# Kernel optimization log

Hardware: AMD Instinct MI355X
Metric: run time of the kernel (lower is better)

The kernel has to match this reference:

```python
import jax, jax.numpy as jnp
import numpy as np

N_NODES = 10000
N_EDGES = 320000
D_IN = 256
D_OUT = 256


def setup_inputs() -> dict:
    key = jax.random.key(0)
    k1, k2, k3, k4, k5, k6 = jax.random.split(key, 6)
    feat = jax.random.normal(k1, (N_NODES, D_IN), dtype=jnp.float32)
    eweight = jax.random.uniform(k2, (N_EDGES, 1), dtype=jnp.float32)
    # Linear(in_dim*2 -> out_dim): weight [out, 2*in], bias [out]
    W = jax.random.normal(k3, (D_OUT, 2 * D_IN), dtype=jnp.float32) / np.sqrt(2 * D_IN)
    b = jax.random.normal(k4, (D_OUT,), dtype=jnp.float32) * 0.01
    src = jax.random.randint(k5, (N_EDGES,), 0, N_NODES, dtype=jnp.int64)
    dst = jax.random.randint(k6, (N_EDGES,), 0, N_NODES, dtype=jnp.int64)
    return {"feat": feat, "eweight": eweight, "W": W, "b": b, "src": src, "dst": dst}


def reference(feat, eweight, W, b, src, dst):
    n = feat.shape[0]
    # message: u_mul_e -> h[src] * ew   (broadcast [E,1] over [E,D])
    msg = feat[src] * eweight
    # mean reduce by destination: sum(msg) / in-degree
    agg = jax.ops.segment_sum(msg, dst, num_segments=n)
    deg = jax.ops.segment_sum(jnp.ones((src.shape[0],), dtype=feat.dtype), dst, num_segments=n)
    h_neigh = agg / jnp.maximum(deg, 1.0)[:, None]
    # concat aggregated with self features, then linear
    h = jnp.concatenate([h_neigh, feat], axis=-1)  # [N, 2*D]
    return h @ W.T + b
```

## Files before the change

kernel.cpp:

```cpp
#include <hip/hip_runtime.h>
#include <hip/hip_bf16.h>

#define N_NODES 10000
#define N_EDGES 320000
#define D 256
#define K_TOT 512
#define CAP 128

typedef __attribute__((ext_vector_type(8))) short bf16x8;
typedef __attribute__((ext_vector_type(4))) float f32x4;

__device__ __forceinline__ float bf2f(unsigned short u) {
  return __uint_as_float(((unsigned int)u) << 16);
}
__device__ __forceinline__ unsigned short f2bf(float f) {
  unsigned int x = __float_as_uint(f);
  unsigned int r = (x + 0x7fffu + ((x >> 16) & 1u)) >> 16;
  return (unsigned short)r;
}

#define FEAT_VECS (N_NODES * D / 8)
#define W_VECS    (D * K_TOT / 8)
#define CUR_VECS  (N_NODES / 4)
__global__ __launch_bounds__(256) void tobf16_kernel(
    const float* __restrict__ feat, const float* __restrict__ W,
    unsigned short* __restrict__ hcat, unsigned short* __restrict__ Wb,
    int* __restrict__ cursor) {
  int gid = blockIdx.x * 256 + threadIdx.x;
  const float* srcp;
  unsigned short* dstp;
  if (gid < FEAT_VECS) {
    int row = gid >> 5;
    int v = gid & 31;
    srcp = feat + (size_t)row * D + v * 8;
    dstp = hcat + (size_t)row * K_TOT + D + v * 8;
  } else if (gid < FEAT_VECS + W_VECS) {
    int g = gid - FEAT_VECS;
    int row = g >> 6;
    int v = g & 63;
    srcp = W + (size_t)row * K_TOT + v * 8;
    dstp = Wb + (size_t)row * K_TOT + v * 8;
  } else if (gid < FEAT_VECS + W_VECS + CUR_VECS) {
    int g = gid - (FEAT_VECS + W_VECS);
    reinterpret_cast<int4*>(cursor)[g] = make_int4(0, 0, 0, 0);
    return;
  } else {
    return;
  }
  float4 a = reinterpret_cast<const float4*>(srcp)[0];
  float4 b = reinterpret_cast<const float4*>(srcp)[1];
  ushort4 o0 = make_ushort4(f2bf(a.x), f2bf(a.y), f2bf(a.z), f2bf(a.w));
  ushort4 o1 = make_ushort4(f2bf(b.x), f2bf(b.y), f2bf(b.z), f2bf(b.w));
  reinterpret_cast<ushort4*>(dstp)[0] = o0;
  reinterpret_cast<ushort4*>(dstp)[1] = o1;
}

__global__ __launch_bounds__(256) void append_kernel(const int* __restrict__ src,
                                                     const int* __restrict__ dst,
                                                     const float* __restrict__ ew,
                                                     int* __restrict__ cursor,
                                                     int2* __restrict__ bucket) {
  int i = blockIdx.x * 256 + threadIdx.x;
  if (i < N_EDGES) {
    int d = dst[i];
    int pos = atomicAdd(&cursor[d], 1);
    if (pos < CAP)
      bucket[(size_t)d * CAP + pos] = make_int2(src[i], __float_as_int(ew[i]));
  }
}

__global__ __launch_bounds__(256) void agg_kernel(const int* __restrict__ cursor,
                                                  const int2* __restrict__ bucket,
                                                  unsigned short* __restrict__ hcat) {
  int node = (blockIdx.x * 256 + threadIdx.x) >> 6;
  int lane = threadIdx.x & 63;
  if (node >= N_NODES) return;
  int cnt = cursor[node];
  int end = min(cnt, CAP);
  const int2* bk = bucket + (size_t)node * CAP;
  float acc0 = 0.f, acc1 = 0.f, acc2 = 0.f, acc3 = 0.f;
  int i = 0;
  for (; i + 4 <= end; i += 4) {
    int4 e01 = *reinterpret_cast<const int4*>(bk + i);
    int4 e23 = *reinterpret_cast<const int4*>(bk + i + 2);
    ushort4 v0 = *reinterpret_cast<const ushort4*>(hcat + (size_t)e01.x * K_TOT + D + lane * 4);
    ushort4 v1 = *reinterpret_cast<const ushort4*>(hcat + (size_t)e01.z * K_TOT + D + lane * 4);
    ushort4 v2 = *reinterpret_cast<const ushort4*>(hcat + (size_t)e23.x * K_TOT + D + lane * 4);
    ushort4 v3 = *reinterpret_cast<const ushort4*>(hcat + (size_t)e23.z * K_TOT + D + lane * 4);
    float w0 = __int_as_float(e01.y), w1 = __int_as_float(e01.w);
    float w2 = __int_as_float(e23.y), w3 = __int_as_float(e23.w);
    acc0 += bf2f(v0.x) * w0; acc1 += bf2f(v0.y) * w0; acc2 += bf2f(v0.z) * w0; acc3 += bf2f(v0.w) * w0;
    acc0 += bf2f(v1.x) * w1; acc1 += bf2f(v1.y) * w1; acc2 += bf2f(v1.z) * w1; acc3 += bf2f(v1.w) * w1;
    acc0 += bf2f(v2.x) * w2; acc1 += bf2f(v2.y) * w2; acc2 += bf2f(v2.z) * w2; acc3 += bf2f(v2.w) * w2;
    acc0 += bf2f(v3.x) * w3; acc1 += bf2f(v3.y) * w3; acc2 += bf2f(v3.z) * w3; acc3 += bf2f(v3.w) * w3;
  }
  for (; i < end; ++i) {
    int2 sw = bk[i];
    ushort4 v = *reinterpret_cast<const ushort4*>(hcat + (size_t)sw.x * K_TOT + D + lane * 4);
    float w = __int_as_float(sw.y);
    acc0 += bf2f(v.x) * w; acc1 += bf2f(v.y) * w; acc2 += bf2f(v.z) * w; acc3 += bf2f(v.w) * w;
  }
  float inv = 1.0f / fmaxf((float)cnt, 1.0f);
  ushort4 o = make_ushort4(f2bf(acc0 * inv), f2bf(acc1 * inv),
                           f2bf(acc2 * inv), f2bf(acc3 * inv));
  *reinterpret_cast<ushort4*>(hcat + (size_t)node * K_TOT + lane * 4) = o;
}

#define GBM 128
#define GBN 64
#define GBK 64
#define LPAD 72

__global__ __launch_bounds__(256) void gemm_kernel(
    const unsigned short* __restrict__ hcat, const unsigned short* __restrict__ Wb,
    const float* __restrict__ bias, float* __restrict__ out) {
  __shared__ unsigned short As[GBM][LPAD];
  __shared__ unsigned short Bs[GBN][LPAD];

  int row0 = blockIdx.x * GBM;
  int col0 = blockIdx.y * GBN;
  int t = threadIdx.x;
  int lane = t & 63;
  int w = t >> 6;
  int wr = w >> 1;
  int wc = w & 1;
  int lhi = lane >> 4;
  int llo = lane & 15;

  f32x4 acc[4][2];
  #pragma unroll
  for (int m = 0; m < 4; ++m)
    #pragma unroll
    for (int n = 0; n < 2; ++n) acc[m][n] = (f32x4){0.f, 0.f, 0.f, 0.f};

  for (int k0 = 0; k0 < K_TOT; k0 += GBK) {
    #pragma unroll
    for (int it = 0; it < 4; ++it) {
      int idx = t + it * 256;
      int r = idx >> 3;
      int kv = (idx & 7) * 8;
      int row = row0 + r;
      uint4 v = make_uint4(0, 0, 0, 0);
      if (row < N_NODES)
        v = *reinterpret_cast<const uint4*>(hcat + (size_t)row * K_TOT + k0 + kv);
      *reinterpret_cast<uint4*>(&As[r][kv]) = v;
    }
    #pragma unroll
    for (int it = 0; it < 2; ++it) {
      int idx = t + it * 256;
      int c = idx >> 3;
      int kv = (idx & 7) * 8;
      uint4 v = *reinterpret_cast<const uint4*>(Wb + (size_t)(col0 + c) * K_TOT + k0 + kv);
      *reinterpret_cast<uint4*>(&Bs[c][kv]) = v;
    }
    __syncthreads();

    #pragma unroll
    for (int ks = 0; ks < 2; ++ks) {
      int ak = ks * 32 + lhi * 8;
      bf16x8 a[4], b[2];
      #pragma unroll
      for (int m = 0; m < 4; ++m)
        a[m] = *reinterpret_cast<const bf16x8*>(&As[wr * 64 + m * 16 + llo][ak]);
      #pragma unroll
      for (int n = 0; n < 2; ++n)
        b[n] = *reinterpret_cast<const bf16x8*>(&Bs[wc * 32 + n * 16 + llo][ak]);
      #pragma unroll
      for (int m = 0; m < 4; ++m)
        #pragma unroll
        for (int n = 0; n < 2; ++n)
          acc[m][n] = __builtin_amdgcn_mfma_f32_16x16x32_bf16(a[m], b[n], acc[m][n], 0, 0, 0);
    }
    __syncthreads();
  }

  #pragma unroll
  for (int m = 0; m < 4; ++m) {
    #pragma unroll
    for (int n = 0; n < 2; ++n) {
      int col = col0 + wc * 32 + n * 16 + llo;
      float bv = bias[col];
      #pragma unroll
      for (int r = 0; r < 4; ++r) {
        int orow = row0 + wr * 64 + m * 16 + lhi * 4 + r;
        if (orow < N_NODES)
          out[(size_t)orow * D + col] = acc[m][n][r] + bv;
      }
    }
  }
}

extern "C" void kernel_launch(void* const* d_in, const int* in_sizes, int n_in,
                              void* d_out, int out_size, void* d_ws, size_t ws_size,
                              hipStream_t stream) {
  const float* feat = (const float*)d_in[0];
  const float* ew   = (const float*)d_in[1];
  const float* W    = (const float*)d_in[2];
  const float* bias = (const float*)d_in[3];
  const int*   src  = (const int*)d_in[4];
  const int*   dst  = (const int*)d_in[5];
  float* out = (float*)d_out;

  char* ws = (char*)d_ws;
  unsigned short* hcat = (unsigned short*)ws;  ws += (size_t)N_NODES * K_TOT * sizeof(unsigned short);
  unsigned short* Wb   = (unsigned short*)ws;  ws += (size_t)D * K_TOT * sizeof(unsigned short);
  int* cursor   = (int*)ws;                    ws += N_NODES * sizeof(int);
  int2* bucket  = (int2*)ws;                   ws += (size_t)N_NODES * CAP * sizeof(int2);

  tobf16_kernel<<<(FEAT_VECS + W_VECS + CUR_VECS + 255) / 256, 256, 0, stream>>>(
      feat, W, hcat, Wb, cursor);
  append_kernel<<<(N_EDGES + 255) / 256, 256, 0, stream>>>(src, dst, ew, cursor, bucket);
  agg_kernel<<<(N_NODES * 64 + 255) / 256, 256, 0, stream>>>(cursor, bucket, hcat);

  dim3 grid((N_NODES + GBM - 1) / GBM, D / GBN);
  gemm_kernel<<<grid, 256, 0, stream>>>(hcat, Wb, bias, out);
}
```

Baseline: 76.92 us.

## Fuse all four stages into one cooperative persistent kernel with grid syncs

Replaces the four separate launches (bf16 conversion, edge bucketing, aggregation, GEMM) with a single cooperative kernel of 628 blocks. The blocks loop over each stage in grid-stride fashion and call grid.sync between stages. The GEMM tile shrinks to 64x64 so that 157x4 tiles map one-to-one onto the blocks. The goal is to remove per-launch overhead and the gaps between kernels. The cost is grid-wide barriers, occupancy limits on the persistent grid (launch bounds of 3 blocks), and a smaller GEMM tile with less reuse.

```diff
diff --git a/kernel.cpp b/kernel.cpp
--- a/kernel.cpp
+++ b/kernel.cpp
@@ -1,5 +1,8 @@
 #include <hip/hip_runtime.h>
 #include <hip/hip_bf16.h>
+#include <hip/hip_cooperative_groups.h>
+
+namespace cg = cooperative_groups;
 
 #define N_NODES 10000
 #define N_EDGES 320000
@@ -7,6 +10,9 @@
 #define K_TOT 512
 #define CAP 128
 
+#define GRID_BLKS 628
+#define NTHREADS (GRID_BLKS * 256)
+
 typedef __attribute__((ext_vector_type(8))) short bf16x8;
 typedef __attribute__((ext_vector_type(4))) float f32x4;
 
@@ -22,169 +28,177 @@
 #define FEAT_VECS (N_NODES * D / 8)
 #define W_VECS    (D * K_TOT / 8)
 #define CUR_VECS  (N_NODES / 4)
-__global__ __launch_bounds__(256) void tobf16_kernel(
-    const float* __restrict__ feat, const float* __restrict__ W,
+#define P0_TOT    (FEAT_VECS + W_VECS + CUR_VECS)
+
+#define GBM 64
+#define GBN 64
+#define GBK 64
+#define LPAD 72
+#define MTILES 157
+
+__global__ __launch_bounds__(256, 3) void fused_kernel(
+    const float* __restrict__ feat, const float* __restrict__ ew,
+    const float* __restrict__ W, const float* __restrict__ bias,
+    const int* __restrict__ src, const int* __restrict__ dst,
     unsigned short* __restrict__ hcat, unsigned short* __restrict__ Wb,
-    int* __restrict__ cursor) {
-  int gid = blockIdx.x * 256 + threadIdx.x;
-  const float* srcp;
-  unsigned short* dstp;
-  if (gid < FEAT_VECS) {
-    int row = gid >> 5;
-    int v = gid & 31;
-    srcp = feat + (size_t)row * D + v * 8;
-    dstp = hcat + (size_t)row * K_TOT + D + v * 8;
-  } else if (gid < FEAT_VECS + W_VECS) {
-    int g = gid - FEAT_VECS;
-    int row = g >> 6;
-    int v = g & 63;
-    srcp = W + (size_t)row * K_TOT + v * 8;
-    dstp = Wb + (size_t)row * K_TOT + v * 8;
-  } else if (gid < FEAT_VECS + W_VECS + CUR_VECS) {
-    int g = gid - (FEAT_VECS + W_VECS);
-    reinterpret_cast<int4*>(cursor)[g] = make_int4(0, 0, 0, 0);
-    return;
-  } else {
-    return;
-  }
-  float4 a = reinterpret_cast<const float4*>(srcp)[0];
-  float4 b = reinterpret_cast<const float4*>(srcp)[1];
-  ushort4 o0 = make_ushort4(f2bf(a.x), f2bf(a.y), f2bf(a.z), f2bf(a.w));
-  ushort4 o1 = make_ushort4(f2bf(b.x), f2bf(b.y), f2bf(b.z), f2bf(b.w));
-  reinterpret_cast<ushort4*>(dstp)[0] = o0;
-  reinterpret_cast<ushort4*>(dstp)[1] = o1;
-}
-
-__global__ __launch_bounds__(256) void append_kernel(const int* __restrict__ src,
-                                                     const int* __restrict__ dst,
-                                                     const float* __restrict__ ew,
-                                                     int* __restrict__ cursor,
-                                                     int2* __restrict__ bucket) {
-  int i = blockIdx.x * 256 + threadIdx.x;
-  if (i < N_EDGES) {
+    int* __restrict__ cursor, int2* __restrict__ bucket,
+    float* __restrict__ out) {
+  __shared__ unsigned short As[GBM][LPAD];
+  __shared__ unsigned short Bs[GBN][LPAD];
+
+  cg::grid_group grid = cg::this_grid();
+  const int tid = blockIdx.x * 256 + threadIdx.x;
+
+  for (int gid = tid; gid < P0_TOT; gid += NTHREADS) {
+    if (gid < FEAT_VECS) {
+      int row = gid >> 5;
+      int v = gid & 31;
+      const float* srcp = feat + (size_t)row * D + v * 8;
+      unsigned short* dstp = hcat + (size_t)row * K_TOT + D + v * 8;
+      float4 a = reinterpret_cast<const float4*>(srcp)[0];
+      float4 b = reinterpret_cast<const float4*>(srcp)[1];
+      reinterpret_cast<ushort4*>(dstp)[0] =
+          make_ushort4(f2bf(a.x), f2bf(a.y), f2bf(a.z), f2bf(a.w));
+      reinterpret_cast<ushort4*>(dstp)[1] =
+          make_ushort4(f2bf(b.x), f2bf(b.y), f2bf(b.z), f2bf(b.w));
+    } else if (gid < FEAT_VECS + W_VECS) {
+      int g = gid - FEAT_VECS;
+      int row = g >> 6;
+      int v = g & 63;
+      const float* srcp = W + (size_t)row * K_TOT + v * 8;
+      unsigned short* dstp = Wb + (size_t)row * K_TOT + v * 8;
+      float4 a = reinterpret_cast<const float4*>(srcp)[0];
+      float4 b = reinterpret_cast<const float4*>(srcp)[1];
+      reinterpret_cast<ushort4*>(dstp)[0] =
+          make_ushort4(f2bf(a.x), f2bf(a.y), f2bf(a.z), f2bf(a.w));
+      reinterpret_cast<ushort4*>(dstp)[1] =
+          make_ushort4(f2bf(b.x), f2bf(b.y), f2bf(b.z), f2bf(b.w));
+    } else {
+      int g = gid - (FEAT_VECS + W_VECS);
+      reinterpret_cast<int4*>(cursor)[g] = make_int4(0, 0, 0, 0);
+    }
+  }
+  grid.sync();
+
+  for (int i = tid; i < N_EDGES; i += NTHREADS) {
     int d = dst[i];
     int pos = atomicAdd(&cursor[d], 1);
     if (pos < CAP)
       bucket[(size_t)d * CAP + pos] = make_int2(src[i], __float_as_int(ew[i]));
   }
-}
-
-__global__ __launch_bounds__(256) void agg_kernel(const int* __restrict__ cursor,
-                                                  const int2* __restrict__ bucket,
-                                                  unsigned short* __restrict__ hcat) {
-  int node = (blockIdx.x * 256 + threadIdx.x) >> 6;
-  int lane = threadIdx.x & 63;
-  if (node >= N_NODES) return;
-  int cnt = cursor[node];
-  int end = min(cnt, CAP);
-  const int2* bk = bucket + (size_t)node * CAP;
-  float acc0 = 0.f, acc1 = 0.f, acc2 = 0.f, acc3 = 0.f;
-  int i = 0;
-  for (; i + 4 <= end; i += 4) {
-    int4 e01 = *reinterpret_cast<const int4*>(bk + i);
-    int4 e23 = *reinterpret_cast<const int4*>(bk + i + 2);
-    ushort4 v0 = *reinterpret_cast<const ushort4*>(hcat + (size_t)e01.x * K_TOT + D + lane * 4);
-    ushort4 v1 = *reinterpret_cast<const ushort4*>(hcat + (size_t)e01.z * K_TOT + D + lane * 4);
-    ushort4 v2 = *reinterpret_cast<const ushort4*>(hcat + (size_t)e23.x * K_TOT + D + lane * 4);
-    ushort4 v3 = *reinterpret_cast<const ushort4*>(hcat + (size_t)e23.z * K_TOT + D + lane * 4);
-    float w0 = __int_as_float(e01.y), w1 = __int_as_float(e01.w);
-    float w2 = __int_as_float(e23.y), w3 = __int_as_float(e23.w);
-    acc0 += bf2f(v0.x) * w0; acc1 += bf2f(v0.y) * w0; acc2 += bf2f(v0.z) * w0; acc3 += bf2f(v0.w) * w0;
-    acc0 += bf2f(v1.x) * w1; acc1 += bf2f(v1.y) * w1; acc2 += bf2f(v1.z) * w1; acc3 += bf2f(v1.w) * w1;
-    acc0 += bf2f(v2.x) * w2; acc1 += bf2f(v2.y) * w2; acc2 += bf2f(v2.z) * w2; acc3 += bf2f(v2.w) * w2;
-    acc0 += bf2f(v3.x) * w3; acc1 += bf2f(v3.y) * w3; acc2 += bf2f(v3.z) * w3; acc3 += bf2f(v3.w) * w3;
-  }
-  for (; i < end; ++i) {
-    int2 sw = bk[i];
-    ushort4 v = *reinterpret_cast<const ushort4*>(hcat + (size_t)sw.x * K_TOT + D + lane * 4);
-    float w = __int_as_float(sw.y);
-    acc0 += bf2f(v.x) * w; acc1 += bf2f(v.y) * w; acc2 += bf2f(v.z) * w; acc3 += bf2f(v.w) * w;
-  }
-  float inv = 1.0f / fmaxf((float)cnt, 1.0f);
-  ushort4 o = make_ushort4(f2bf(acc0 * inv), f2bf(acc1 * inv),
-                           f2bf(acc2 * inv), f2bf(acc3 * inv));
-  *reinterpret_cast<ushort4*>(hcat + (size_t)node * K_TOT + lane * 4) = o;
-}
-
-#define GBM 128
-#define GBN 64
-#define GBK 64
-#define LPAD 72
-
-__global__ __launch_bounds__(256) void gemm_kernel(
-    const unsigned short* __restrict__ hcat, const unsigned short* __restrict__ Wb,
-    const float* __restrict__ bias, float* __restrict__ out) {
-  __shared__ unsigned short As[GBM][LPAD];
-  __shared__ unsigned short Bs[GBN][LPAD];
-
-  int row0 = blockIdx.x * GBM;
-  int col0 = blockIdx.y * GBN;
-  int t = threadIdx.x;
-  int lane = t & 63;
-  int w = t >> 6;
-  int wr = w >> 1;
-  int wc = w & 1;
-  int lhi = lane >> 4;
-  int llo = lane & 15;
-
-  f32x4 acc[4][2];
-  #pragma unroll
-  for (int m = 0; m < 4; ++m)
+  grid.sync();
+
+  {
+    int wid = tid >> 6;
+    int lane = tid & 63;
+    const int NW = NTHREADS >> 6;
+    for (int node = wid; node < N_NODES; node += NW) {
+      int cnt = cursor[node];
+      int end = min(cnt, CAP);
+      const int2* bk = bucket + (size_t)node * CAP;
+      float acc0 = 0.f, acc1 = 0.f, acc2 = 0.f, acc3 = 0.f;
+      int i = 0;
+      for (; i + 4 <= end; i += 4) {
+        int4 e01 = *reinterpret_cast<const int4*>(bk + i);
+        int4 e23 = *reinterpret_cast<const int4*>(bk + i + 2);
+        ushort4 v0 = *reinterpret_cast<const ushort4*>(hcat + (size_t)e01.x * K_TOT + D + lane * 4);
+        ushort4 v1 = *reinterpret_cast<const ushort4*>(hcat + (size_t)e01.z * K_TOT + D + lane * 4);
+        ushort4 v2 = *reinterpret_cast<const ushort4*>(hcat + (size_t)e23.x * K_TOT + D + lane * 4);
+        ushort4 v3 = *reinterpret_cast<const ushort4*>(hcat + (size_t)e23.z * K_TOT + D + lane * 4);
+        float w0 = __int_as_float(e01.y), w1 = __int_as_float(e01.w);
+        float w2 = __int_as_float(e23.y), w3 = __int_as_float(e23.w);
+        acc0 += bf2f(v0.x) * w0; acc1 += bf2f(v0.y) * w0; acc2 += bf2f(v0.z) * w0; acc3 += bf2f(v0.w) * w0;
+        acc0 += bf2f(v1.x) * w1; acc1 += bf2f(v1.y) * w1; acc2 += bf2f(v1.z) * w1; acc3 += bf2f(v1.w) * w1;
+        acc0 += bf2f(v2.x) * w2; acc1 += bf2f(v2.y) * w2; acc2 += bf2f(v2.z) * w2; acc3 += bf2f(v2.w) * w2;
+        acc0 += bf2f(v3.x) * w3; acc1 += bf2f(v3.y) * w3; acc2 += bf2f(v3.z) * w3; acc3 += bf2f(v3.w) * w3;
+      }
+      for (; i < end; ++i) {
+        int2 sw = bk[i];
+        ushort4 v = *reinterpret_cast<const ushort4*>(hcat + (size_t)sw.x * K_TOT + D + lane * 4);
+        float w = __int_as_float(sw.y);
+        acc0 += bf2f(v.x) * w; acc1 += bf2f(v.y) * w; acc2 += bf2f(v.z) * w; acc3 += bf2f(v.w) * w;
+      }
+      float inv = 1.0f / fmaxf((float)cnt, 1.0f);
+      ushort4 o = make_ushort4(f2bf(acc0 * inv), f2bf(acc1 * inv),
+                               f2bf(acc2 * inv), f2bf(acc3 * inv));
+      *reinterpret_cast<ushort4*>(hcat + (size_t)node * K_TOT + lane * 4) = o;
+    }
+  }
+  grid.sync();
+
+  {
+    int bid = blockIdx.x;
+    int trow = bid % MTILES;
+    int tcol = bid / MTILES;
+    int row0 = trow * GBM;
+    int col0 = tcol * GBN;
+    int t = threadIdx.x;
+    int lane = t & 63;
+    int w = t >> 6;
+    int wr = w >> 1;
+    int wc = w & 1;
+    int lhi = lane >> 4;
+    int llo = lane & 15;
+
+    f32x4 acc[2][2];
     #pragma unroll
-    for (int n = 0; n < 2; ++n) acc[m][n] = (f32x4){0.f, 0.f, 0.f, 0.f};
-
-  for (int k0 = 0; k0 < K_TOT; k0 += GBK) {
+    for (int m = 0; m < 2; ++m)
+      #pragma unroll
+      for (int n = 0; n < 2; ++n) acc[m][n] = (f32x4){0.f, 0.f, 0.f, 0.f};
+
+    for (int k0 = 0; k0 < K_TOT; k0 += GBK) {
+      #pragma unroll
+      for (int it = 0; it < 2; ++it) {
+        int idx = t + it * 256;
+        int r = idx >> 3;
+        int kv = (idx & 7) * 8;
+        int row = row0 + r;
+        uint4 v = make_uint4(0, 0, 0, 0);
+        if (row < N_NODES)
+          v = *reinterpret_cast<const uint4*>(hcat + (size_t)row * K_TOT + k0 + kv);
+        *reinterpret_cast<uint4*>(&As[r][kv]) = v;
+      }
+      #pragma unroll
+      for (int it = 0; it < 2; ++it) {
+        int idx = t + it * 256;
+        int c = idx >> 3;
+        int kv = (idx & 7) * 8;
+        uint4 v = *reinterpret_cast<const uint4*>(Wb + (size_t)(col0 + c) * K_TOT + k0 + kv);
+        *reinterpret_cast<uint4*>(&Bs[c][kv]) = v;
+      }
+      __syncthreads();
+
+      #pragma unroll
+      for (int ks = 0; ks < 2; ++ks) {
+        int ak = ks * 32 + lhi * 8;
+        bf16x8 a[2], b[2];
+        #pragma unroll
+        for (int m = 0; m < 2; ++m)
+          a[m] = *reinterpret_cast<const bf16x8*>(&As[wr * 32 + m * 16 + llo][ak]);
+        #pragma unroll
+        for (int n = 0; n < 2; ++n)
+          b[n] = *reinterpret_cast<const bf16x8*>(&Bs[wc * 32 + n * 16 + llo][ak]);
+        #pragma unroll
+        for (int m = 0; m < 2; ++m)
+          #pragma unroll
+          for (int n = 0; n < 2; ++n)
+            acc[m][n] = __builtin_amdgcn_mfma_f32_16x16x32_bf16(a[m], b[n], acc[m][n], 0, 0, 0);
+      }
+      __syncthreads();
+    }
+
     #pragma unroll
-    for (int it = 0; it < 4; ++it) {
-      int idx = t + it * 256;
-      int r = idx >> 3;
-      int kv = (idx & 7) * 8;
-      int row = row0 + r;
-      uint4 v = make_uint4(0, 0, 0, 0);
-      if (row < N_NODES)
-        v = *reinterpret_cast<const uint4*>(hcat + (size_t)row * K_TOT + k0 + kv);
-      *reinterpret_cast<uint4*>(&As[r][kv]) = v;
-    }
-    #pragma unroll
-    for (int it = 0; it < 2; ++it) {
-      int idx = t + it * 256;
-      int c = idx >> 3;
-      int kv = (idx & 7) * 8;
-      uint4 v = *reinterpret_cast<const uint4*>(Wb + (size_t)(col0 + c) * K_TOT + k0 + kv);
-      *reinterpret_cast<uint4*>(&Bs[c][kv]) = v;
-    }
-    __syncthreads();
-
-    #pragma unroll
-    for (int ks = 0; ks < 2; ++ks) {
-      int ak = ks * 32 + lhi * 8;
-      bf16x8 a[4], b[2];
-      #pragma unroll
-      for (int m = 0; m < 4; ++m)
-        a[m] = *reinterpret_cast<const bf16x8*>(&As[wr * 64 + m * 16 + llo][ak]);
-      #pragma unroll
-      for (int n = 0; n < 2; ++n)
-        b[n] = *reinterpret_cast<const bf16x8*>(&Bs[wc * 32 + n * 16 + llo][ak]);
-      #pragma unroll
-      for (int m = 0; m < 4; ++m)
-        #pragma unroll
-        for (int n = 0; n < 2; ++n)
-          acc[m][n] = __builtin_amdgcn_mfma_f32_16x16x32_bf16(a[m], b[n], acc[m][n], 0, 0, 0);
-    }
-    __syncthreads();
-  }
-
-  #pragma unroll
-  for (int m = 0; m < 4; ++m) {
-    #pragma unroll
-    for (int n = 0; n < 2; ++n) {
-      int col = col0 + wc * 32 + n * 16 + llo;
-      float bv = bias[col];
-      #pragma unroll
-      for (int r = 0; r < 4; ++r) {
-        int orow = row0 + wr * 64 + m * 16 + lhi * 4 + r;
-        if (orow < N_NODES)
-          out[(size_t)orow * D + col] = acc[m][n][r] + bv;
+    for (int m = 0; m < 2; ++m) {
+      #pragma unroll
+      for (int n = 0; n < 2; ++n) {
+        int col = col0 + wc * 32 + n * 16 + llo;
+        float bv = bias[col];
+        #pragma unroll
+        for (int r = 0; r < 4; ++r) {
+          int orow = row0 + wr * 32 + m * 16 + lhi * 4 + r;
+          if (orow < N_NODES)
+            out[(size_t)orow * D + col] = acc[m][n][r] + bv;
+        }
       }
     }
   }
@@ -207,11 +221,11 @@
   int* cursor   = (int*)ws;                    ws += N_NODES * sizeof(int);
   int2* bucket  = (int2*)ws;                   ws += (size_t)N_NODES * CAP * sizeof(int2);
 
-  tobf16_kernel<<<(FEAT_VECS + W_VECS + CUR_VECS + 255) / 256, 256, 0, stream>>>(
-      feat, W, hcat, Wb, cursor);
-  append_kernel<<<(N_EDGES + 255) / 256, 256, 0, stream>>>(src, dst, ew, cursor, bucket);
-  agg_kernel<<<(N_NODES * 64 + 255) / 256, 256, 0, stream>>>(cursor, bucket, hcat);
-
-  dim3 grid((N_NODES + GBM - 1) / GBM, D / GBN);
-  gemm_kernel<<<grid, 256, 0, stream>>>(hcat, Wb, bias, out);
-}
+  void* args[] = {
+      (void*)&feat, (void*)&ew, (void*)&W, (void*)&bias,
+      (void*)&src, (void*)&dst,
+      (void*)&hcat, (void*)&Wb, (void*)&cursor, (void*)&bucket,
+      (void*)&out};
+  hipLaunchCooperativeKernel((void*)fused_kernel, dim3(GRID_BLKS), dim3(256),
+                             args, 0, stream);
+}
```

Result: slower. 294.7 us (+283.1%).
